# Kernel optimization log

Hardware: AMD Instinct MI355X
Metric: run time of the kernel (lower is better)

## Reference

```python
import jax, jax.numpy as jnp
import numpy as np

H = 64  # hidden_size

def _lstm_layer(x_tbf, W_ih, W_hh, b_ih, b_hh):
    # x_tbf: [T, B, F]; W_ih: [4H, F]; W_hh: [4H, H]; biases: [4H]
    T, B, _ = x_tbf.shape
    # precompute input projections for all timesteps at once: [T, B, 4H]
    x_proj = jnp.einsum('tbf,gf->tbg', x_tbf, W_ih) + (b_ih + b_hh)

    def step(carry, xp):
        h, c = carry
        gates = xp + h @ W_hh.T  # [B, 4H]
        i, f, g, o = jnp.split(gates, 4, axis=-1)
        i = jax.nn.sigmoid(i)
        f = jax.nn.sigmoid(f)
        g = jnp.tanh(g)
        o = jax.nn.sigmoid(o)
        c = f * c + i * g
        h = o * jnp.tanh(c)
        return (h, c), h

    h0 = jnp.zeros((B, H), dtype=x_tbf.dtype)
    c0 = jnp.zeros((B, H), dtype=x_tbf.dtype)
    (_, _), hs = jax.lax.scan(step, (h0, c0), x_proj)
    return hs  # [T, B, H]


def setup_inputs() -> dict:
    key = jax.random.key(0)
    ks = jax.random.split(key, 12)
    B, T, F = 1024, 512, 32
    s_in = 1.0 / np.sqrt(H)  # torch LSTM init scale
    u = lambda k, shape: jax.random.uniform(k, shape, jnp.float32, -s_in, s_in)
    return {
        'x': jax.random.normal(ks[0], (B, T, F), jnp.float32),
        'W_ih0': u(ks[1], (4 * H, F)),
        'W_hh0': u(ks[2], (4 * H, H)),
        'b_ih0': u(ks[3], (4 * H,)),
        'b_hh0': u(ks[4], (4 * H,)),
        'W_ih1': u(ks[5], (4 * H, H)),
        'W_hh1': u(ks[6], (4 * H, H)),
        'b_ih1': u(ks[7], (4 * H,)),
        'b_hh1': u(ks[8], (4 * H,)),
        'fc_w': u(ks[9], (1, H)),
        'fc_b': u(ks[10], (1,)),
    }


def reference(x, W_ih0, W_hh0, b_ih0, b_hh0, W_ih1, W_hh1, b_ih1, b_hh1, fc_w, fc_b):
    # x: [B, T, F] (batch_first); run 2 stacked LSTM layers, take last step, linear head
    x_tbf = jnp.transpose(x, (1, 0, 2))  # [T, B, F]
    h1 = _lstm_layer(x_tbf, W_ih0, W_hh0, b_ih0, b_hh0)  # [T, B, H]
    h2 = _lstm_layer(h1, W_ih1, W_hh1, b_ih1, b_hh1)      # [T, B, H]
    last = h2[-1]                                          # [B, H]
    return last @ fc_w.T + fc_b                            # [B, 1]
```

## Files before the change

### kernel.cpp

```cpp
#include <hip/hip_runtime.h>
#include <math.h>

#define H  64
#define F  32
#define NB 4
#define NT 512
#define HS 80

typedef __attribute__((ext_vector_type(8))) short   s8v;
typedef __attribute__((ext_vector_type(8))) __bf16  bf8v;
typedef __attribute__((ext_vector_type(4))) float   f4v;

__device__ __forceinline__ unsigned short f2bf(float x) {
    unsigned u = __builtin_bit_cast(unsigned, x);
    u += 0x7FFFu + ((u >> 16) & 1u);
    return (unsigned short)(u >> 16);
}
__device__ __forceinline__ unsigned cvtpk(float a, float b) {
    unsigned r;
    asm("v_cvt_pk_bf16_f32 %0, %1, %2" : "=v"(r) : "v"(a), "v"(b));
    return r;
}
__device__ __forceinline__ f4v mfma_(s8v a, s8v b, f4v c) {
    return __builtin_amdgcn_mfma_f32_16x16x32_bf16(
        __builtin_bit_cast(bf8v, a), __builtin_bit_cast(bf8v, b), c, 0, 0, 0);
}
__device__ __forceinline__ float sig_(float x) {
    return __builtin_amdgcn_rcpf(1.0f + __expf(-x));
}
__device__ __forceinline__ float tanh_(float x) {
    return 1.0f - 2.0f * __builtin_amdgcn_rcpf(1.0f + __expf(2.0f * x));
}
__device__ __forceinline__ void bar_lds() {
    asm volatile("s_waitcnt lgkmcnt(0)" ::: "memory");
    __builtin_amdgcn_s_barrier();
}
__device__ __forceinline__ s8v load_hi(const float* __restrict__ Wrow, int koff) {
    s8v hi;
    #pragma unroll
    for (int i = 0; i < 8; ++i) hi[i] = (short)f2bf(Wrow[koff + i]);
    return hi;
}
__device__ __forceinline__ s8v xfrag(const float4& a, const float4& b) {
    s8v r; unsigned* ru = (unsigned*)&r;
    ru[0] = cvtpk(a.x, a.y); ru[1] = cvtpk(a.z, a.w);
    ru[2] = cvtpk(b.x, b.y); ru[3] = cvtpk(b.z, b.w);
    return r;
}

__global__ __launch_bounds__(NT, 2)
void lstm_v13(const float* __restrict__ x,
              const float* __restrict__ Wih0,
              const float* __restrict__ Whh0,
              const float* __restrict__ bih0,
              const float* __restrict__ bhh0,
              const float* __restrict__ Wih1,
              const float* __restrict__ Whh1,
              const float* __restrict__ bih1,
              const float* __restrict__ bhh1,
              const float* __restrict__ fcw,
              const float* __restrict__ fcb,
              float* __restrict__ out,
              int T, int B)
{
    const int tid  = threadIdx.x;
    const int w    = tid >> 6;
    const int wl   = w & 3;
    const bool isL0 = (w < 4);
    const int lane = tid & 63;
    const int j    = lane & 15;
    const int hi4  = lane >> 4;
    const int bm   = j >> 2;
    const int u    = 16 * wl + j;
    const int b0   = blockIdx.x * NB;

    __shared__ alignas(16) unsigned short h0[2][NB][HS];
    __shared__ alignas(16) unsigned short h1[2][NB][HS];
    __shared__ float part[4][64];

    for (int i = tid; i < 2 * NB * HS; i += NT) {
        (&h0[0][0][0])[i] = 0;
        (&h1[0][0][0])[i] = 0;
    }

    if (isL0) {
        s8v wxh[4];
        s8v whh[4][2];
        float bias[4];
        #pragma unroll
        for (int g = 0; g < 4; ++g) {
            const int R = 64 * g + 16 * wl + j;
            wxh[g] = load_hi(&Wih0[R * F], 8 * hi4);
            whh[g][0] = load_hi(&Whh0[R * H], 8 * hi4);
            whh[g][1] = load_hi(&Whh0[R * H], 32 + 8 * hi4);
            bias[g] = bih0[R] + bhh0[R];
        }
        const float* xrow = x + ((size_t)(b0 + bm) * T) * F + 8 * hi4;
        const int tmax = T - 1;
        float4 p0 = *(const float4*)(xrow);
        float4 p1 = *(const float4*)(xrow + 4);
        s8v xf = xfrag(p0, p1);
        const size_t o1 = (size_t)((1 < tmax) ? 1 : tmax) * F;
        const size_t o2 = (size_t)((2 < tmax) ? 2 : tmax) * F;
        float4 xB0 = *(const float4*)(xrow + o1), xB1 = *(const float4*)(xrow + o1 + 4);
        float4 xA0 = *(const float4*)(xrow + o2), xA1 = *(const float4*)(xrow + o2 + 4);

        __syncthreads();

        float c = 0.f;
        f4v accA[4], accB[4];

        auto phA = [&](int s, int par) {
            if (s < T) {
                const s8v hf0 = *(const s8v*)&h0[par ^ 1][bm][8 * hi4];
                const s8v hf1 = *(const s8v*)&h0[par ^ 1][bm][8 * (4 + hi4)];
                __builtin_amdgcn_s_setprio(1);
                #pragma unroll
                for (int g = 0; g < 4; ++g) {
                    f4v av = {bias[g], bias[g], bias[g], bias[g]};
                    accA[g] = mfma_(xf, wxh[g], av);
                    f4v bv = {0.f, 0.f, 0.f, 0.f};
                    bv = mfma_(hf0, whh[g][0], bv);
                    accB[g] = mfma_(hf1, whh[g][1], bv);
                }
                __builtin_amdgcn_s_setprio(0);
            }
            bar_lds();
        };
        auto phB = [&](int s, int par, float4& n0, float4& n1) {
            if (s < T) {
                const float gi = sig_(accA[0][0] + accB[0][0]);
                const float gf = sig_(accA[1][0] + accB[1][0]);
                const float gg = tanh_(accA[2][0] + accB[2][0]);
                const float go = sig_(accA[3][0] + accB[3][0]);
                c = gf * c + gi * gg;
                const float hv = go * tanh_(c);
                h0[par][hi4][u] = (unsigned short)cvtpk(hv, hv);
                xf = xfrag(n0, n1);
                const size_t tld = (size_t)((s + 3 < tmax) ? (s + 3) : tmax) * F;
                n0 = *(const float4*)(xrow + tld);
                n1 = *(const float4*)(xrow + tld + 4);
            }
            bar_lds();
        };

        #pragma unroll 1
        for (int s = 0; s < T + 2; s += 2) {
            phA(s, 0);     phB(s, 0, xB0, xB1);
            phA(s + 1, 1); phB(s + 1, 1, xA0, xA1);
        }
    } else {
        s8v wgh[4][2];
        s8v whh[4][2];
        float bias[4];
        #pragma unroll
        for (int g = 0; g < 4; ++g) {
            const int R = 64 * g + 16 * wl + j;
            wgh[g][0] = load_hi(&Wih1[R * H], 8 * hi4);
            wgh[g][1] = load_hi(&Wih1[R * H], 32 + 8 * hi4);
            whh[g][0] = load_hi(&Whh1[R * H], 8 * hi4);
            whh[g][1] = load_hi(&Whh1[R * H], 32 + 8 * hi4);
            bias[g] = bih1[R] + bhh1[R];
        }
        const float fcwr = fcw[u];
        __syncthreads();

        float c = 0.f;
        f4v accA[4], accB[4];

        #pragma unroll 1
        for (int s = 0; s <= T + 1; ++s) {
            const int par = s & 1;
            s8v gf0 = {}, gf1 = {};
            if (s >= 1 && s <= T) {
                gf0 = *(const s8v*)&h0[par ^ 1][bm][8 * hi4];
                gf1 = *(const s8v*)&h0[par ^ 1][bm][8 * (4 + hi4)];
            }
            if (s >= 2) {
                const float gi = sig_(accA[0][0] + accB[0][0]);
                const float gf = sig_(accA[1][0] + accB[1][0]);
                const float gg = tanh_(accA[2][0] + accB[2][0]);
                const float go = sig_(accA[3][0] + accB[3][0]);
                c = gf * c + gi * gg;
                const float hv = go * tanh_(c);
                if (s <= T) {
                    h1[par][hi4][u] = (unsigned short)cvtpk(hv, hv);
                } else {
                    part[wl][lane] = hv * fcwr;
                }
            }
            bar_lds();
            if (s >= 1 && s <= T) {
                const s8v hf0 = *(const s8v*)&h1[par][bm][8 * hi4];
                const s8v hf1 = *(const s8v*)&h1[par][bm][8 * (4 + hi4)];
                __builtin_amdgcn_s_setprio(1);
                #pragma unroll
                for (int g = 0; g < 4; ++g) {
                    f4v av = {bias[g], bias[g], bias[g], bias[g]};
                    av = mfma_(gf0, wgh[g][0], av);
                    accA[g] = mfma_(gf1, wgh[g][1], av);
                    f4v bv = {0.f, 0.f, 0.f, 0.f};
                    bv = mfma_(hf0, whh[g][0], bv);
                    accB[g] = mfma_(hf1, whh[g][1], bv);
                }
                __builtin_amdgcn_s_setprio(0);
            }
            bar_lds();
        }
    }

    __syncthreads();

    if (tid < 64) {
        float v = part[0][lane] + part[1][lane] + part[2][lane] + part[3][lane];
        v += __shfl_xor(v, 1);
        v += __shfl_xor(v, 2);
        v += __shfl_xor(v, 4);
        v += __shfl_xor(v, 8);
        if (j == 0) out[b0 + hi4] = v + fcb[0];
    }
}

extern "C" void kernel_launch(void* const* d_in, const int* in_sizes, int n_in,
                              void* d_out, int out_size, void* d_ws, size_t ws_size,
                              hipStream_t stream) {
    const float* x    = (const float*)d_in[0];
    const float* Wih0 = (const float*)d_in[1];
    const float* Whh0 = (const float*)d_in[2];
    const float* bih0 = (const float*)d_in[3];
    const float* bhh0 = (const float*)d_in[4];
    const float* Wih1 = (const float*)d_in[5];
    const float* Whh1 = (const float*)d_in[6];
    const float* bih1 = (const float*)d_in[7];
    const float* bhh1 = (const float*)d_in[8];
    const float* fcw  = (const float*)d_in[9];
    const float* fcb  = (const float*)d_in[10];
    float* out = (float*)d_out;

    const int B = out_size;
    const int T = in_sizes[0] / (B * F);

    dim3 grid(B / NB), block(NT);
    hipLaunchKernelGGL(lstm_v13, grid, block, 0, stream,
                       x, Wih0, Whh0, bih0, bhh0,
                       Wih1, Whh1, bih1, bhh1, fcw, fcb,
                       out, T, B);
}
```

Before: 248.8 us.

## Halve per-step barriers using an LDS counter spin-wait for layer-1 waves

Layer 0 now fuses its MFMA phase and gate/activation phase into one step with a single workgroup barrier, instead of two barriers per timestep. Layer 1 issues its input-projection MFMAs (from h0) before waiting, then synchronises only its own four waves through an LDS atomic counter and spin-loop. It then accumulates the recurrent MFMAs into the same accumulators, using ping-pong accumulator arrays. The aim is to shorten the serial critical path of each timestep by cutting whole-block barrier stalls. The cost is busy-wait spinning and reliance on correct LDS memory ordering between waves.

Result: slower. 298.4 us (+19.9%).

```diff
diff --git a/kernel.cpp b/kernel.cpp
--- a/kernel.cpp
+++ b/kernel.cpp
@@ -49,7 +49,7 @@
 }
 
 __global__ __launch_bounds__(NT, 2)
-void lstm_v13(const float* __restrict__ x,
+void lstm_v14(const float* __restrict__ x,
               const float* __restrict__ Wih0,
               const float* __restrict__ Whh0,
               const float* __restrict__ bih0,
@@ -77,11 +77,13 @@
     __shared__ alignas(16) unsigned short h0[2][NB][HS];
     __shared__ alignas(16) unsigned short h1[2][NB][HS];
     __shared__ float part[4][64];
+    __shared__ int cnt;
 
     for (int i = tid; i < 2 * NB * HS; i += NT) {
         (&h0[0][0][0])[i] = 0;
         (&h1[0][0][0])[i] = 0;
     }
+    if (tid == 0) cnt = 0;
 
     if (isL0) {
         s8v wxh[4];
@@ -108,31 +110,25 @@
         __syncthreads();
 
         float c = 0.f;
-        f4v accA[4], accB[4];
-
-        auto phA = [&](int s, int par) {
+        auto stepL0 = [&](int s, int par, float4& n0, float4& n1) {
             if (s < T) {
                 const s8v hf0 = *(const s8v*)&h0[par ^ 1][bm][8 * hi4];
                 const s8v hf1 = *(const s8v*)&h0[par ^ 1][bm][8 * (4 + hi4)];
                 __builtin_amdgcn_s_setprio(1);
+                f4v a[4], b[4];
                 #pragma unroll
                 for (int g = 0; g < 4; ++g) {
                     f4v av = {bias[g], bias[g], bias[g], bias[g]};
-                    accA[g] = mfma_(xf, wxh[g], av);
+                    a[g] = mfma_(xf, wxh[g], av);
                     f4v bv = {0.f, 0.f, 0.f, 0.f};
                     bv = mfma_(hf0, whh[g][0], bv);
-                    accB[g] = mfma_(hf1, whh[g][1], bv);
+                    b[g] = mfma_(hf1, whh[g][1], bv);
                 }
                 __builtin_amdgcn_s_setprio(0);
-            }
-            bar_lds();
-        };
-        auto phB = [&](int s, int par, float4& n0, float4& n1) {
-            if (s < T) {
-                const float gi = sig_(accA[0][0] + accB[0][0]);
-                const float gf = sig_(accA[1][0] + accB[1][0]);
-                const float gg = tanh_(accA[2][0] + accB[2][0]);
-                const float go = sig_(accA[3][0] + accB[3][0]);
+                const float gi = sig_(a[0][0] + b[0][0]);
+                const float gf = sig_(a[1][0] + b[1][0]);
+                const float gg = tanh_(a[2][0] + b[2][0]);
+                const float go = sig_(a[3][0] + b[3][0]);
                 c = gf * c + gi * gg;
                 const float hv = go * tanh_(c);
                 h0[par][hi4][u] = (unsigned short)cvtpk(hv, hv);
@@ -146,8 +142,8 @@
 
         #pragma unroll 1
         for (int s = 0; s < T + 2; s += 2) {
-            phA(s, 0);     phB(s, 0, xB0, xB1);
-            phA(s + 1, 1); phB(s + 1, 1, xA0, xA1);
+            stepL0(s,     0, xB0, xB1);
+            stepL0(s + 1, 1, xA0, xA1);
         }
     } else {
         s8v wgh[4][2];
@@ -166,21 +162,26 @@
         __syncthreads();
 
         float c = 0.f;
-        f4v accA[4], accB[4];
-
-        #pragma unroll 1
-        for (int s = 0; s <= T + 1; ++s) {
-            const int par = s & 1;
-            s8v gf0 = {}, gf1 = {};
+        f4v accP[4], accQ[4];
+
+        auto stepL1 = [&](int s, int par, f4v (&aN)[4], f4v (&aO)[4]) {
             if (s >= 1 && s <= T) {
-                gf0 = *(const s8v*)&h0[par ^ 1][bm][8 * hi4];
-                gf1 = *(const s8v*)&h0[par ^ 1][bm][8 * (4 + hi4)];
+                const s8v gf0 = *(const s8v*)&h0[par ^ 1][bm][8 * hi4];
+                const s8v gf1 = *(const s8v*)&h0[par ^ 1][bm][8 * (4 + hi4)];
+                __builtin_amdgcn_s_setprio(1);
+                #pragma unroll
+                for (int g = 0; g < 4; ++g) {
+                    f4v av = {bias[g], bias[g], bias[g], bias[g]};
+                    av = mfma_(gf0, wgh[g][0], av);
+                    aN[g] = mfma_(gf1, wgh[g][1], av);
+                }
+                __builtin_amdgcn_s_setprio(0);
             }
             if (s >= 2) {
-                const float gi = sig_(accA[0][0] + accB[0][0]);
-                const float gf = sig_(accA[1][0] + accB[1][0]);
-                const float gg = tanh_(accA[2][0] + accB[2][0]);
-                const float go = sig_(accA[3][0] + accB[3][0]);
+                const float gi = sig_(aO[0][0]);
+                const float gf = sig_(aO[1][0]);
+                const float gg = tanh_(aO[2][0]);
+                const float go = sig_(aO[3][0]);
                 c = gf * c + gi * gg;
                 const float hv = go * tanh_(c);
                 if (s <= T) {
@@ -189,23 +190,33 @@
                     part[wl][lane] = hv * fcwr;
                 }
             }
-            bar_lds();
+            if (s >= 2 && s <= T) {
+                asm volatile("s_waitcnt lgkmcnt(0)" ::: "memory");
+                if (lane == 0) atomicAdd(&cnt, 1);
+                const int tgt = 4 * (s - 1);
+                volatile int* p = &cnt;
+                while (*p < tgt) {}
+                __builtin_amdgcn_sched_barrier(0);
+                asm volatile("" ::: "memory");
+            }
             if (s >= 1 && s <= T) {
                 const s8v hf0 = *(const s8v*)&h1[par][bm][8 * hi4];
                 const s8v hf1 = *(const s8v*)&h1[par][bm][8 * (4 + hi4)];
                 __builtin_amdgcn_s_setprio(1);
                 #pragma unroll
                 for (int g = 0; g < 4; ++g) {
-                    f4v av = {bias[g], bias[g], bias[g], bias[g]};
-                    av = mfma_(gf0, wgh[g][0], av);
-                    accA[g] = mfma_(gf1, wgh[g][1], av);
-                    f4v bv = {0.f, 0.f, 0.f, 0.f};
-                    bv = mfma_(hf0, whh[g][0], bv);
-                    accB[g] = mfma_(hf1, whh[g][1], bv);
+                    aN[g] = mfma_(hf0, whh[g][0], aN[g]);
+                    aN[g] = mfma_(hf1, whh[g][1], aN[g]);
                 }
                 __builtin_amdgcn_s_setprio(0);
             }
             bar_lds();
+        };
+
+        #pragma unroll 1
+        for (int s = 0; s < T + 2; s += 2) {
+            stepL1(s,     0, accP, accQ);
+            stepL1(s + 1, 1, accQ, accP);
         }
     }
 
@@ -241,7 +252,7 @@
     const int T = in_sizes[0] / (B * F);
 
     dim3 grid(B / NB), block(NT);
-    hipLaunchKernelGGL(lstm_v13, grid, block, 0, stream,
+    hipLaunchKernelGGL(lstm_v14, grid, block, 0, stream,
                        x, Wih0, Whh0, bih0, bhh0,
                        Wih1, Whh1, bih1, bhh1, fcw, fcb,
                        out, T, B);
```
